# Optimization experiments

Measured on AMD Instinct MI355X. Metric: run time of the kernel, lower is better.

Reference implementation:

```python
import jax, jax.numpy as jnp
import numpy as np


def setup_inputs() -> dict:
    key = jax.random.key(0)
    k1, k2, k3, k4 = jax.random.split(key, 4)
    B, L, K, E, V = 32, 256, 8, 768, 50000
    hidden_feature = jax.random.normal(k1, (B, L, E), dtype=jnp.float32)
    similar_words_sent = jax.random.randint(k2, (B, L, K), 0, V, dtype=jnp.int64)
    word2vec = jax.random.normal(k3, (V, E), dtype=jnp.float32)
    # xavier_uniform for (E, E)
    limit = float(np.sqrt(6.0 / (E + E)))
    weight = jax.random.uniform(k4, (E, E), dtype=jnp.float32, minval=-limit, maxval=limit)
    return {
        "hidden_feature": hidden_feature,
        "similar_words_sent": similar_words_sent,
        "word2vec": word2vec,
        "weight": weight,
    }


def reference(hidden_feature, similar_words_sent, word2vec, weight):
    # Gather k similar-word embeddings: [B, L, K, E]
    k_sims = word2vec[similar_words_sent]
    # Bilinear attention scores: (q @ W) . k  -> [B, L, K]
    q_proj = jnp.einsum("ble,ef->blf", hidden_feature, weight)
    scores = jnp.einsum("ble,blke->blk", q_proj, k_sims)
    attn = jax.nn.softmax(scores, axis=-1)
    # Dropout is identity in eval / rate 0.
    out = jnp.einsum("blk,blke->ble", attn, k_sims)
    return out
```

## Files before the change

kernel.cpp:

```cpp
#include <hip/hip_runtime.h>
#include <hip/hip_bf16.h>


typedef __attribute__((ext_vector_type(8))) _Float16 f16x8;
typedef __attribute__((ext_vector_type(4))) float f32x4;

__device__ __forceinline__ unsigned short f2h(float f) {
    _Float16 h = (_Float16)f;
    return __builtin_bit_cast(unsigned short, h);
}

__device__ __forceinline__ void gload16(const void* g, void* l) {
    __builtin_amdgcn_global_load_lds(
        (const __attribute__((address_space(1))) unsigned int*)g,
        (__attribute__((address_space(3))) unsigned int*)l, 16, 0, 0);
}

__global__ __launch_bounds__(256) void split_all(const float4* __restrict__ x,
                                                 ushort4* __restrict__ hf, int n4,
                                                 const float* __restrict__ W,
                                                 unsigned short* __restrict__ WfT,
                                                 int K, int N, int ablocks) {
    __shared__ float tile[32][33];
    if ((int)blockIdx.x < ablocks) {
        int i = blockIdx.x * 256 + threadIdx.x;
        const int stride = ablocks * 256;
        for (; i < n4; i += stride) {
            float4 v = x[i];
            ushort4 h;
            h.x = f2h(v.x); h.y = f2h(v.y); h.z = f2h(v.z); h.w = f2h(v.w);
            hf[i] = h;
        }
    } else {
        const int bid = blockIdx.x - ablocks;
        const int nbk = K / 32;
        const int bk = (bid % nbk) * 32, bn = (bid / nbk) * 32;
        const int tx = threadIdx.x & 31, ty = threadIdx.x >> 5;
#pragma unroll
        for (int r = ty; r < 32; r += 8)
            tile[r][tx] = W[(size_t)(bk + r) * N + bn + tx];
        __syncthreads();
#pragma unroll
        for (int r = ty; r < 32; r += 8) {
            float v = tile[tx][r];
            WfT[(size_t)(bn + r) * K + bk + tx] = f2h(v);
        }
    }
}


#define BM 128
#define BN 64
#define BK 64

__global__ __launch_bounds__(512, 6) void gemm_mfma_f16(
        const unsigned short* __restrict__ Af, const unsigned short* __restrict__ BfT,
        float* __restrict__ C, int M, int N, int K) {

    const int nwg = gridDim.x;
    const int per = nwg >> 3;
    const int l   = (blockIdx.x & 7) * per + (blockIdx.x >> 3);
    const int nbn = N / BN;
    const int bm  = (l / nbn) * BM;
    const int bn  = (l % nbn) * BN;

    __shared__ unsigned short lds[1536 * 8];
    const int BOFF = 1024;

    const int tid  = threadIdx.x;
    const int lane = tid & 63;
    const int w    = tid >> 6;
    const int lr   = lane & 15, lg = lane >> 4;
    const int wm   = w >> 1, wn = w & 1;

    const int lane8 = lane >> 3;
    const int kcl   = (lane & 7) ^ lane8;

    f32x4 acc[2][2];
#pragma unroll
    for (int m = 0; m < 2; ++m)
#pragma unroll
        for (int n = 0; n < 2; ++n) acc[m][n] = (f32x4){0.f, 0.f, 0.f, 0.f};

    const int niter = K / BK;
    for (int it = 0; it < niter; ++it) {
        const int k0 = it * BK;

#pragma unroll
        for (int i = 0; i < 2; ++i) {
            size_t g = (size_t)(bm + 16 * w + 8 * i + lane8) * K + k0 + kcl * 8;
            gload16(Af + g, &lds[(size_t)(128 * w + 64 * i) * 8]);
        }
        {
            size_t g = (size_t)(bn + 8 * w + lane8) * K + k0 + kcl * 8;
            gload16(BfT + g, &lds[(size_t)(BOFF + 64 * w) * 8]);
        }
        __syncthreads();

#pragma unroll
        for (int ks = 0; ks < 2; ++ks) {
            const int kc = ks * 4 + lg;
            const int kx = kc ^ (lr & 7);
            f16x8 a[2], b[2];
#pragma unroll
            for (int m = 0; m < 2; ++m) {
                int slot = (wm * 32 + m * 16 + lr) * 8 + kx;
                a[m] = *(const f16x8*)&lds[(size_t)slot * 8];
            }
#pragma unroll
            for (int n = 0; n < 2; ++n) {
                int slot = (wn * 32 + n * 16 + lr) * 8 + kx;
                b[n] = *(const f16x8*)&lds[(size_t)(BOFF + slot) * 8];
            }
#pragma unroll
            for (int m = 0; m < 2; ++m)
#pragma unroll
                for (int n = 0; n < 2; ++n)
                    acc[m][n] = __builtin_amdgcn_mfma_f32_16x16x32_f16(a[m], b[n], acc[m][n], 0, 0, 0);
        }
        __syncthreads();
    }

#pragma unroll
    for (int m = 0; m < 2; ++m)
#pragma unroll
        for (int n = 0; n < 2; ++n) {
            const int col = bn + wn * 32 + n * 16 + lr;
            const int r0  = bm + wm * 32 + m * 16 + lg * 4;
#pragma unroll
            for (int j = 0; j < 4; ++j)
                C[(size_t)(r0 + j) * N + col] = acc[m][n][j];
        }
}

#define GM_BM 128
#define GM_BN 64
#define GM_BK 16
#define GM_TM 8
#define GM_TN 4

__global__ __launch_bounds__(256) void gemm_qproj(const float* __restrict__ A,
                                                  const float* __restrict__ B,
                                                  float* __restrict__ C,
                                                  int M, int N, int K) {
    __shared__ float As[GM_BK][GM_BM];
    __shared__ float Bs[GM_BK][GM_BN];
    const int tid = threadIdx.x;
    const int tx = tid & 15;
    const int ty = tid >> 4;
    const int bm = blockIdx.x * GM_BM;
    const int bn = blockIdx.y * GM_BN;
    float acc[GM_TM][GM_TN];
#pragma unroll
    for (int i = 0; i < GM_TM; ++i)
#pragma unroll
        for (int j = 0; j < GM_TN; ++j) acc[i][j] = 0.f;
    for (int k0 = 0; k0 < K; k0 += GM_BK) {
#pragma unroll
        for (int i = 0; i < 2; ++i) {
            int idx = tid * 2 + i;
            int row = idx >> 2;
            int c4  = idx & 3;
            float4 v = *(const float4*)(A + (size_t)(bm + row) * K + k0 + c4 * 4);
            As[c4 * 4 + 0][row] = v.x;
            As[c4 * 4 + 1][row] = v.y;
            As[c4 * 4 + 2][row] = v.z;
            As[c4 * 4 + 3][row] = v.w;
        }
        {
            int row = tid >> 4;
            int c4  = tid & 15;
            float4 v = *(const float4*)(B + (size_t)(k0 + row) * N + bn + c4 * 4);
            *(float4*)&Bs[row][c4 * 4] = v;
        }
        __syncthreads();
#pragma unroll
        for (int k = 0; k < GM_BK; ++k) {
            float a[GM_TM], b[GM_TN];
#pragma unroll
            for (int i = 0; i < GM_TM; ++i) a[i] = As[k][ty * GM_TM + i];
#pragma unroll
            for (int j = 0; j < GM_TN; ++j) b[j] = Bs[k][tx * GM_TN + j];
#pragma unroll
            for (int i = 0; i < GM_TM; ++i)
#pragma unroll
                for (int j = 0; j < GM_TN; ++j) acc[i][j] += a[i] * b[j];
        }
        __syncthreads();
    }
#pragma unroll
    for (int i = 0; i < GM_TM; ++i) {
        float4 v;
        v.x = acc[i][0]; v.y = acc[i][1]; v.z = acc[i][2]; v.w = acc[i][3];
        *(float4*)(C + (size_t)(bm + ty * GM_TM + i) * N + bn + tx * GM_TN) = v;
    }
}

__global__ __launch_bounds__(256) void attn_fused(const float* __restrict__ qproj,
                                                  const int* __restrict__ sws,
                                                  const float* __restrict__ w2v,
                                                  float* __restrict__ out) {
    const int wave = threadIdx.x >> 6;
    const int lane = threadIdx.x & 63;
    const size_t row = (size_t)blockIdx.x * 4 + wave;

    const float4* q4 = (const float4*)(qproj + row * 768);
    float4 q[3];
#pragma unroll
    for (int j = 0; j < 3; ++j) q[j] = q4[j * 64 + lane];

    float4 ks[8][3];
    float dot[8];
#pragma unroll
    for (int k = 0; k < 8; ++k) {
        int id = sws[row * 8 + k];
        const float4* kp = (const float4*)(w2v + (size_t)id * 768);
        float d = 0.f;
#pragma unroll
        for (int j = 0; j < 3; ++j) {
            float4 v = kp[j * 64 + lane];
            ks[k][j] = v;
            d += q[j].x * v.x;
            d += q[j].y * v.y;
            d += q[j].z * v.z;
            d += q[j].w * v.w;
        }
        dot[k] = d;
    }
#pragma unroll
    for (int k = 0; k < 8; ++k) {
        float d = dot[k];
#pragma unroll
        for (int m = 1; m < 64; m <<= 1) d += __shfl_xor(d, m);
        dot[k] = d;
    }
    float mx = dot[0];
#pragma unroll
    for (int k = 1; k < 8; ++k) mx = fmaxf(mx, dot[k]);
    float w[8];
    float s = 0.f;
#pragma unroll
    for (int k = 0; k < 8; ++k) { w[k] = __expf(dot[k] - mx); s += w[k]; }
    const float inv = 1.f / s;

    float4 o[3];
#pragma unroll
    for (int j = 0; j < 3; ++j) { o[j].x = 0.f; o[j].y = 0.f; o[j].z = 0.f; o[j].w = 0.f; }
#pragma unroll
    for (int k = 0; k < 8; ++k) {
        const float a = w[k] * inv;
#pragma unroll
        for (int j = 0; j < 3; ++j) {
            o[j].x += a * ks[k][j].x;
            o[j].y += a * ks[k][j].y;
            o[j].z += a * ks[k][j].z;
            o[j].w += a * ks[k][j].w;
        }
    }
    float4* o4 = (float4*)(out + row * 768);
#pragma unroll
    for (int j = 0; j < 3; ++j) o4[j * 64 + lane] = o[j];
}

extern "C" void kernel_launch(void* const* d_in, const int* in_sizes, int n_in,
                              void* d_out, int out_size, void* d_ws, size_t ws_size,
                              hipStream_t stream) {
    const float* hidden = (const float*)d_in[0];
    const int*   sws    = (const int*)d_in[1];
    const float* w2v    = (const float*)d_in[2];
    const float* weight = (const float*)d_in[3];
    float*       out    = (float*)d_out;

    const int E = 768;
    const int M = in_sizes[0] / E;
    float* qproj = out;

    const size_t szA = (size_t)M * E * sizeof(unsigned short);
    const size_t szB = (size_t)E * E * sizeof(unsigned short);
    const size_t need = szA + szB;

    if (ws_size >= need) {
        unsigned short* Af  = (unsigned short*)d_ws;
        unsigned short* WfT = Af + (size_t)M * E;

        const int ablocks = 2048;
        const int wblocks = (E / 32) * (E / 32);
        split_all<<<ablocks + wblocks, 256, 0, stream>>>(
            (const float4*)hidden, (ushort4*)Af, M * E / 4,
            weight, WfT, E, E, ablocks);

        dim3 ggrid((M / BM) * (E / BN));
        gemm_mfma_f16<<<ggrid, 512, 0, stream>>>(Af, WfT, qproj, M, E, E);
    } else {
        dim3 ggrid(M / GM_BM, E / GM_BN);
        gemm_qproj<<<ggrid, 256, 0, stream>>>(hidden, weight, qproj, M, E, E);
    }

    attn_fused<<<dim3(M / 4), 256, 0, stream>>>(qproj, sws, w2v, out);
}
```

Before: 64.98 us.

## Double-buffer MFMA GEMM with larger per-wave tiles and fp16 q_proj output

```diff
diff --git a/kernel.cpp b/kernel.cpp
--- a/kernel.cpp
+++ b/kernel.cpp
@@ -8,6 +8,9 @@
 __device__ __forceinline__ unsigned short f2h(float f) {
     _Float16 h = (_Float16)f;
     return __builtin_bit_cast(unsigned short, h);
+}
+__device__ __forceinline__ float h2f(unsigned short u) {
+    return (float)__builtin_bit_cast(_Float16, u);
 }
 
 __device__ __forceinline__ void gload16(const void* g, void* l) {
@@ -53,9 +56,9 @@
 #define BN 64
 #define BK 64
 
-__global__ __launch_bounds__(512, 6) void gemm_mfma_f16(
+__global__ __launch_bounds__(256) void gemm_mfma_f16(
         const unsigned short* __restrict__ Af, const unsigned short* __restrict__ BfT,
-        float* __restrict__ C, int M, int N, int K) {
+        unsigned short* __restrict__ C, int M, int N, int K) {
 
     const int nwg = gridDim.x;
     const int per = nwg >> 3;
@@ -64,8 +67,9 @@
     const int bm  = (l / nbn) * BM;
     const int bn  = (l % nbn) * BN;
 
-    __shared__ unsigned short lds[1536 * 8];
+    __shared__ unsigned short lds[2 * 1536 * 8];
     const int BOFF = 1024;
+    const int BUF  = 1536;
 
     const int tid  = threadIdx.x;
     const int lane = tid & 63;
@@ -76,60 +80,68 @@
     const int lane8 = lane >> 3;
     const int kcl   = (lane & 7) ^ lane8;
 
-    f32x4 acc[2][2];
-#pragma unroll
-    for (int m = 0; m < 2; ++m)
+    f32x4 acc[4][2];
+#pragma unroll
+    for (int m = 0; m < 4; ++m)
 #pragma unroll
         for (int n = 0; n < 2; ++n) acc[m][n] = (f32x4){0.f, 0.f, 0.f, 0.f};
 
+    auto STAGE = [&](int k0, int buf) {
+#pragma unroll
+        for (int i = 0; i < 4; ++i) {
+            size_t g = (size_t)(bm + 32 * w + 8 * i + lane8) * K + k0 + kcl * 8;
+            gload16(Af + g, &lds[(size_t)(buf * BUF + 256 * w + 64 * i) * 8]);
+        }
+#pragma unroll
+        for (int i = 0; i < 2; ++i) {
+            size_t g = (size_t)(bn + 16 * w + 8 * i + lane8) * K + k0 + kcl * 8;
+            gload16(BfT + g, &lds[(size_t)(buf * BUF + BOFF + 128 * w + 64 * i) * 8]);
+        }
+    };
+
     const int niter = K / BK;
+    STAGE(0, 0);
+    __syncthreads();
+
+    int cur = 0;
     for (int it = 0; it < niter; ++it) {
-        const int k0 = it * BK;
-
-#pragma unroll
-        for (int i = 0; i < 2; ++i) {
-            size_t g = (size_t)(bm + 16 * w + 8 * i + lane8) * K + k0 + kcl * 8;
-            gload16(Af + g, &lds[(size_t)(128 * w + 64 * i) * 8]);
-        }
-        {
-            size_t g = (size_t)(bn + 8 * w + lane8) * K + k0 + kcl * 8;
-            gload16(BfT + g, &lds[(size_t)(BOFF + 64 * w) * 8]);
-        }
-        __syncthreads();
-
+        if (it + 1 < niter) STAGE((it + 1) * BK, cur ^ 1);
+
+        const int base = cur * BUF;
 #pragma unroll
         for (int ks = 0; ks < 2; ++ks) {
             const int kc = ks * 4 + lg;
             const int kx = kc ^ (lr & 7);
-            f16x8 a[2], b[2];
-#pragma unroll
-            for (int m = 0; m < 2; ++m) {
-                int slot = (wm * 32 + m * 16 + lr) * 8 + kx;
+            f16x8 a[4], b[2];
+#pragma unroll
+            for (int m = 0; m < 4; ++m) {
+                int slot = base + (wm * 64 + m * 16 + lr) * 8 + kx;
                 a[m] = *(const f16x8*)&lds[(size_t)slot * 8];
             }
 #pragma unroll
             for (int n = 0; n < 2; ++n) {
-                int slot = (wn * 32 + n * 16 + lr) * 8 + kx;
-                b[n] = *(const f16x8*)&lds[(size_t)(BOFF + slot) * 8];
+                int slot = base + BOFF + (wn * 32 + n * 16 + lr) * 8 + kx;
+                b[n] = *(const f16x8*)&lds[(size_t)slot * 8];
             }
 #pragma unroll
-            for (int m = 0; m < 2; ++m)
+            for (int m = 0; m < 4; ++m)
 #pragma unroll
                 for (int n = 0; n < 2; ++n)
                     acc[m][n] = __builtin_amdgcn_mfma_f32_16x16x32_f16(a[m], b[n], acc[m][n], 0, 0, 0);
         }
         __syncthreads();
-    }
-
-#pragma unroll
-    for (int m = 0; m < 2; ++m)
+        cur ^= 1;
+    }
+
+#pragma unroll
+    for (int m = 0; m < 4; ++m)
 #pragma unroll
         for (int n = 0; n < 2; ++n) {
             const int col = bn + wn * 32 + n * 16 + lr;
-            const int r0  = bm + wm * 32 + m * 16 + lg * 4;
+            const int r0  = bm + wm * 64 + m * 16 + lg * 4;
 #pragma unroll
             for (int j = 0; j < 4; ++j)
-                C[(size_t)(r0 + j) * N + col] = acc[m][n][j];
+                C[(size_t)(r0 + j) * N + col] = f2h(acc[m][n][j]);
         }
 }
 
@@ -196,6 +208,75 @@
     }
 }
 
+__global__ __launch_bounds__(256) void attn_fused_h(const unsigned short* __restrict__ qf,
+                                                    const int* __restrict__ sws,
+                                                    const float* __restrict__ w2v,
+                                                    float* __restrict__ out) {
+    const int wave = threadIdx.x >> 6;
+    const int lane = threadIdx.x & 63;
+    const size_t row = (size_t)blockIdx.x * 4 + wave;
+
+    const ushort4* q4 = (const ushort4*)(qf + row * 768);
+    float4 q[3];
+#pragma unroll
+    for (int j = 0; j < 3; ++j) {
+        ushort4 h = q4[j * 64 + lane];
+        q[j].x = h2f(h.x); q[j].y = h2f(h.y); q[j].z = h2f(h.z); q[j].w = h2f(h.w);
+    }
+
+    float4 ks[8][3];
+    float dot[8];
+#pragma unroll
+    for (int k = 0; k < 8; ++k) {
+        int id = sws[row * 8 + k];
+        const float4* kp = (const float4*)(w2v + (size_t)id * 768);
+        float d = 0.f;
+#pragma unroll
+        for (int j = 0; j < 3; ++j) {
+            float4 v = kp[j * 64 + lane];
+            ks[k][j] = v;
+            d += q[j].x * v.x;
+            d += q[j].y * v.y;
+            d += q[j].z * v.z;
+            d += q[j].w * v.w;
+        }
+        dot[k] = d;
+    }
+#pragma unroll
+    for (int k = 0; k < 8; ++k) {
+        float d = dot[k];
+#pragma unroll
+        for (int m = 1; m < 64; m <<= 1) d += __shfl_xor(d, m);
+        dot[k] = d;
+    }
+    float mx = dot[0];
+#pragma unroll
+    for (int k = 1; k < 8; ++k) mx = fmaxf(mx, dot[k]);
+    float w[8];
+    float s = 0.f;
+#pragma unroll
+    for (int k = 0; k < 8; ++k) { w[k] = __expf(dot[k] - mx); s += w[k]; }
+    const float inv = 1.f / s;
+
+    float4 o[3];
+#pragma unroll
+    for (int j = 0; j < 3; ++j) { o[j].x = 0.f; o[j].y = 0.f; o[j].z = 0.f; o[j].w = 0.f; }
+#pragma unroll
+    for (int k = 0; k < 8; ++k) {
+        const float a = w[k] * inv;
+#pragma unroll
+        for (int j = 0; j < 3; ++j) {
+            o[j].x += a * ks[k][j].x;
+            o[j].y += a * ks[k][j].y;
+            o[j].z += a * ks[k][j].z;
+            o[j].w += a * ks[k][j].w;
+        }
+    }
+    float4* o4 = (float4*)(out + row * 768);
+#pragma unroll
+    for (int j = 0; j < 3; ++j) o4[j * 64 + lane] = o[j];
+}
+
 __global__ __launch_bounds__(256) void attn_fused(const float* __restrict__ qproj,
                                                   const int* __restrict__ sws,
                                                   const float* __restrict__ w2v,
@@ -220,10 +301,7 @@
         for (int j = 0; j < 3; ++j) {
             float4 v = kp[j * 64 + lane];
             ks[k][j] = v;
-            d += q[j].x * v.x;
-            d += q[j].y * v.y;
-            d += q[j].z * v.z;
-            d += q[j].w * v.w;
+            d += q[j].x * v.x + q[j].y * v.y + q[j].z * v.z + q[j].w * v.w;
         }
         dot[k] = d;
     }
@@ -273,15 +351,15 @@
 
     const int E = 768;
     const int M = in_sizes[0] / E;
-    float* qproj = out;
-
-    const size_t szA = (size_t)M * E * sizeof(unsigned short);
-    const size_t szB = (size_t)E * E * sizeof(unsigned short);
-    const size_t need = szA + szB;
+
+    const size_t szA = (size_t)M * E;
+    const size_t szB = (size_t)E * E;
+    const size_t need = (2 * szA + szB) * sizeof(unsigned short);
 
     if (ws_size >= need) {
         unsigned short* Af  = (unsigned short*)d_ws;
-        unsigned short* WfT = Af + (size_t)M * E;
+        unsigned short* WfT = Af + szA;
+        unsigned short* Qf  = WfT + szB;
 
         const int ablocks = 2048;
         const int wblocks = (E / 32) * (E / 32);
@@ -290,11 +368,13 @@
             weight, WfT, E, E, ablocks);
 
         dim3 ggrid((M / BM) * (E / BN));
-        gemm_mfma_f16<<<ggrid, 512, 0, stream>>>(Af, WfT, qproj, M, E, E);
+        gemm_mfma_f16<<<ggrid, 256, 0, stream>>>(Af, WfT, Qf, M, E, E);
+
+        attn_fused_h<<<dim3(M / 4), 256, 0, stream>>>(Qf, sws, w2v, out);
     } else {
+        float* qproj = out;
         dim3 ggrid(M / GM_BM, E / GM_BN);
         gemm_qproj<<<ggrid, 256, 0, stream>>>(hidden, weight, qproj, M, E, E);
-    }
-
-    attn_fused<<<dim3(M / 4), 256, 0, stream>>>(qproj, sws, w2v, out);
-}
+        attn_fused<<<dim3(M / 4), 256, 0, stream>>>(qproj, sws, w2v, out);
+    }
+}
```

Measured after the change: 63.62 us. 1.02x faster.
